# Performance work log

Hardware: AMD Instinct MI355X
Metric: run time of the kernel (lower is better)

Reference implementation:

```python
import jax, jax.numpy as jnp
import numpy as np

N_NODES = 50000
N_EDGES = 800000
D_FEAT = 64


def setup_inputs() -> dict:
    key = jax.random.key(0)
    k1, k2, k3 = jax.random.split(key, 3)
    x_sum = jax.random.normal(k1, (N_NODES, D_FEAT), dtype=jnp.float32)
    x_prod = jax.random.uniform(k2, (N_NODES, D_FEAT), dtype=jnp.float32)
    edge_index = jax.random.randint(k3, (2, N_EDGES), 0, N_NODES, dtype=jnp.int64)
    return {"x_sum": x_sum, "x_prod": x_prod, "edge_index": edge_index}


def reference(x_sum, x_prod, edge_index):
    # flow='source_to_target' -> gather from edge_index[0], aggregate at edge_index[1]
    src_idx = edge_index[0]
    dst_idx = edge_index[1]
    n = x_sum.shape[0]

    # __lift__: index_select along node dim (message is identity; edge_attr/norm None)
    m_sum = x_sum[src_idx]    # [E, D]
    m_prod = x_prod[src_idx]  # [E, D]

    # scatter_sum: zeros-init + scatter_add_
    out_sum = jax.ops.segment_sum(m_sum, dst_idx, num_segments=n)

    # scatter_product: ones-init + scatter_(reduce='multiply')
    out_prod = jnp.ones((n, x_prod.shape[1]), dtype=x_prod.dtype).at[dst_idx].multiply(m_prod)

    return out_sum, out_prod
```

## Files before the change

### kernel.cpp

```cpp
#include <hip/hip_runtime.h>
#include <hip/hip_fp16.h>

#define N_NODES 50000
#define N_EDGES 800000
#define D_FEAT  64
#define BSHIFT  6
#define NBKT    782
#define NB      256
#define CHUNK   3125
#define PSHIFT  20
#define SRC_MASK ((1 << PSHIFT) - 1)

#define WS_FLAG    0
#define WS_TOT     64
#define WS_COFF    (WS_TOT + NBKT)
#define WS_BH      (WS_COFF + NBKT + 1)
#define WS_OFFS    (WS_BH + NBKT * NB)
#define WS_PAIR    (WS_OFFS + N_NODES + 1)
#define WS_SSRC    (WS_PAIR + N_EDGES)
#define WS_PACKED  (WS_SSRC + N_EDGES)
#define WS_INTS    (WS_PACKED + N_NODES * D_FEAT)

__device__ inline void detect_idx_layout(const int* idx, int* flag) {
    int allzero = 1;
    #pragma unroll
    for (int i = 1; i < 129; i += 2) {
        if (idx[i] != 0) allzero = 0;
    }
    *flag = allzero;
}

__global__ __launch_bounds__(256) void init_cast(int* __restrict__ W,
                                                 const int* __restrict__ idx,
                                                 const float* __restrict__ xs,
                                                 const float* __restrict__ xp) {
    int tid = blockIdx.x * blockDim.x + threadIdx.x;
    int stride = gridDim.x * blockDim.x;
    __half2* packed = (__half2*)(W + WS_PACKED);
    const int total = N_NODES * D_FEAT;
    for (int i = tid; i < total; i += stride)
        packed[i] = __floats2half2_rn(xs[i], xp[i]);
    if (tid == 0) {
        detect_idx_layout(idx, W + WS_FLAG);
        W[WS_OFFS + N_NODES] = N_EDGES;
    }
}

__global__ __launch_bounds__(256) void block_hist(const int* __restrict__ idx,
                                                  int* __restrict__ W) {
    __shared__ int h[NBKT];
    for (int i = threadIdx.x; i < NBKT; i += 256) h[i] = 0;
    __syncthreads();
    const int flg = W[WS_FLAG];
    const int base = blockIdx.x * CHUNK;
    for (int e = base + threadIdx.x; e < base + CHUNK; e += 256) {
        int dst = flg ? idx[2 * (N_EDGES + e)] : idx[N_EDGES + e];
        atomicAdd(&h[dst >> BSHIFT], 1);
    }
    __syncthreads();
    for (int i = threadIdx.x; i < NBKT; i += 256)
        W[WS_BH + i * NB + blockIdx.x] = h[i];
}

__global__ __launch_bounds__(256) void bucket_scan(int* __restrict__ W) {
    __shared__ int part[NB];
    int j = blockIdx.x;
    int t = threadIdx.x;
    int c = W[WS_BH + j * NB + t];
    part[t] = c;
    __syncthreads();
    for (int off = 1; off < NB; off <<= 1) {
        int u = (t >= off) ? part[t - off] : 0;
        __syncthreads();
        part[t] += u;
        __syncthreads();
    }
    W[WS_BH + j * NB + t] = part[t] - c;
    if (t == NB - 1) W[WS_TOT + j] = part[t];
}

__global__ __launch_bounds__(1024) void base_scan(int* __restrict__ W) {
    __shared__ int part[1024];
    int t = threadIdx.x;
    int v = (t < NBKT) ? W[WS_TOT + t] : 0;
    part[t] = v;
    __syncthreads();
    for (int off = 1; off < 1024; off <<= 1) {
        int u = (t >= off) ? part[t - off] : 0;
        __syncthreads();
        part[t] += u;
        __syncthreads();
    }
    if (t < NBKT) W[WS_COFF + t] = part[t] - v;
    if (t == 0) W[WS_COFF + NBKT] = N_EDGES;
}

__global__ __launch_bounds__(256) void coarse_scatter(const int* __restrict__ idx,
                                                      int* __restrict__ W) {
    __shared__ int cur[NBKT];
    for (int i = threadIdx.x; i < NBKT; i += 256)
        cur[i] = W[WS_COFF + i] + W[WS_BH + i * NB + blockIdx.x];
    __syncthreads();
    const int flg = W[WS_FLAG];
    const int base = blockIdx.x * CHUNK;
    for (int e = base + threadIdx.x; e < base + CHUNK; e += 256) {
        int src, dst;
        if (flg) { src = idx[2 * e]; dst = idx[2 * (N_EDGES + e)]; }
        else     { src = idx[e];     dst = idx[N_EDGES + e]; }
        int pos = atomicAdd(&cur[dst >> BSHIFT], 1);
        W[WS_PAIR + pos] = src | ((dst & 63) << PSHIFT);
    }
}

__global__ __launch_bounds__(256) void fine_sort(int* __restrict__ W) {
    __shared__ int h[64];
    int b = blockIdx.x;
    int t = threadIdx.x;
    int bbase = W[WS_COFF + b];
    int bend  = W[WS_COFF + b + 1];
    if (t < 64) h[t] = 0;
    __syncthreads();
    for (int e = bbase + t; e < bend; e += 256)
        atomicAdd(&h[(unsigned)W[WS_PAIR + e] >> PSHIFT], 1);
    __syncthreads();
    if (t < 64) {
        int c = h[t];
        int incl = c;
        #pragma unroll
        for (int off = 1; off < 64; off <<= 1) {
            int u = __shfl_up(incl, off, 64);
            if (t >= off) incl += u;
        }
        int excl = incl - c;
        int node = (b << BSHIFT) + t;
        if (node < N_NODES) W[WS_OFFS + node] = bbase + excl;
        h[t] = excl;
    }
    __syncthreads();
    for (int e = bbase + t; e < bend; e += 256) {
        int v = W[WS_PAIR + e];
        int p = atomicAdd(&h[(unsigned)v >> PSHIFT], 1);
        W[WS_SSRC + bbase + p] = v & SRC_MASK;
    }
}

__global__ __launch_bounds__(256) void gather_reduce(const int* __restrict__ W,
                                                     float* __restrict__ out) {
    int wave = (int)((blockIdx.x * blockDim.x + threadIdx.x) >> 6);
    int lane = threadIdx.x & 63;
    if (wave >= N_NODES) return;
    int beg = __builtin_amdgcn_readfirstlane(W[WS_OFFS + wave]);
    int end = __builtin_amdgcn_readfirstlane(W[WS_OFFS + wave + 1]);
    const int* ssrc = W + WS_SSRC;
    const __half2* packed = (const __half2*)(W + WS_PACKED);

    float s0 = 0.f, s1 = 0.f, s2 = 0.f, s3 = 0.f;
    float s4 = 0.f, s5 = 0.f, s6 = 0.f, s7 = 0.f;
    float p0 = 1.f, p1 = 1.f, p2 = 1.f, p3 = 1.f;
    float p4 = 1.f, p5 = 1.f, p6 = 1.f, p7 = 1.f;
    int i = beg;
    for (; i + 7 < end; i += 8) {
        int a0 = ssrc[i],     a1 = ssrc[i + 1], a2 = ssrc[i + 2], a3 = ssrc[i + 3];
        int a4 = ssrc[i + 4], a5 = ssrc[i + 5], a6 = ssrc[i + 6], a7 = ssrc[i + 7];
        float2 f0 = __half22float2(packed[a0 * D_FEAT + lane]);
        float2 f1 = __half22float2(packed[a1 * D_FEAT + lane]);
        float2 f2 = __half22float2(packed[a2 * D_FEAT + lane]);
        float2 f3 = __half22float2(packed[a3 * D_FEAT + lane]);
        float2 f4 = __half22float2(packed[a4 * D_FEAT + lane]);
        float2 f5 = __half22float2(packed[a5 * D_FEAT + lane]);
        float2 f6 = __half22float2(packed[a6 * D_FEAT + lane]);
        float2 f7 = __half22float2(packed[a7 * D_FEAT + lane]);
        s0 += f0.x; s1 += f1.x; s2 += f2.x; s3 += f3.x;
        s4 += f4.x; s5 += f5.x; s6 += f6.x; s7 += f7.x;
        p0 *= f0.y; p1 *= f1.y; p2 *= f2.y; p3 *= f3.y;
        p4 *= f4.y; p5 *= f5.y; p6 *= f6.y; p7 *= f7.y;
    }
    for (; i + 1 < end; i += 2) {
        int a0 = ssrc[i], a1 = ssrc[i + 1];
        float2 f0 = __half22float2(packed[a0 * D_FEAT + lane]);
        float2 f1 = __half22float2(packed[a1 * D_FEAT + lane]);
        s0 += f0.x; s1 += f1.x;
        p0 *= f0.y; p1 *= f1.y;
    }
    if (i < end) {
        float2 f = __half22float2(packed[ssrc[i] * D_FEAT + lane]);
        s0 += f.x;
        p0 *= f.y;
    }
    float ssum = ((s0 + s1) + (s2 + s3)) + ((s4 + s5) + (s6 + s7));
    float pprd = ((p0 * p1) * (p2 * p3)) * ((p4 * p5) * (p6 * p7));
    out[(long)wave * D_FEAT + lane] = ssum;
    out[(long)N_NODES * D_FEAT + (long)wave * D_FEAT + lane] = pprd;
}

__device__ inline void atomicMulF32(float* addr, float val) {
    unsigned int* ua = (unsigned int*)addr;
    unsigned int old = __hip_atomic_load(ua, __ATOMIC_RELAXED, __HIP_MEMORY_SCOPE_AGENT);
    while (true) {
        unsigned int assumed = old;
        unsigned int desired = __float_as_uint(__uint_as_float(assumed) * val);
        old = atomicCAS(ua, assumed, desired);
        if (old == assumed) break;
    }
}

__global__ void fb_init(float* __restrict__ out, int* __restrict__ flag,
                        const int* __restrict__ idx) {
    const int n4 = (N_NODES * D_FEAT) / 4;
    int tid = blockIdx.x * blockDim.x + threadIdx.x;
    int stride = gridDim.x * blockDim.x;
    float4* o = (float4*)out;
    const float4 z = make_float4(0.f, 0.f, 0.f, 0.f);
    const float4 one = make_float4(1.f, 1.f, 1.f, 1.f);
    for (int i = tid; i < n4; i += stride) { o[i] = z; o[n4 + i] = one; }
    if (blockIdx.x == 0 && threadIdx.x == 0) detect_idx_layout(idx, flag);
}

__global__ void fb_scatter(const float* __restrict__ xs, const float* __restrict__ xp,
                           const int* __restrict__ idx, float* __restrict__ out,
                           const int* __restrict__ flag) {
    long tid = (long)blockIdx.x * blockDim.x + threadIdx.x;
    const long total = (long)N_EDGES * (D_FEAT / 4);
    if (tid >= total) return;
    int e = (int)(tid >> 4);
    int c = (int)(tid & 15);
    int src, dst;
    if (*flag) { src = idx[2 * e]; dst = idx[2 * (N_EDGES + e)]; }
    else       { src = idx[e];     dst = idx[N_EDGES + e]; }
    const float4 s = ((const float4*)(xs + (long)src * D_FEAT))[c];
    const float4 p = ((const float4*)(xp + (long)src * D_FEAT))[c];
    float* os = out + (long)dst * D_FEAT + c * 4;
    float* op = out + (long)N_NODES * D_FEAT + (long)dst * D_FEAT + c * 4;
    atomicAdd(os + 0, s.x); atomicAdd(os + 1, s.y);
    atomicAdd(os + 2, s.z); atomicAdd(os + 3, s.w);
    atomicMulF32(op + 0, p.x); atomicMulF32(op + 1, p.y);
    atomicMulF32(op + 2, p.z); atomicMulF32(op + 3, p.w);
}

extern "C" void kernel_launch(void* const* d_in, const int* in_sizes, int n_in,
                              void* d_out, int out_size, void* d_ws, size_t ws_size,
                              hipStream_t stream) {
    const float* x_sum  = (const float*)d_in[0];
    const float* x_prod = (const float*)d_in[1];
    const int*   eidx   = (const int*)d_in[2];
    float* out = (float*)d_out;
    int* W = (int*)d_ws;

    if (ws_size < (size_t)WS_INTS * sizeof(int)) {
        fb_init<<<1024, 256, 0, stream>>>(out, W, eidx);
        const long total = (long)N_EDGES * (D_FEAT / 4);
        int grid = (int)((total + 255) / 256);
        fb_scatter<<<grid, 256, 0, stream>>>(x_sum, x_prod, eidx, out, W);
        return;
    }

    init_cast<<<1024, 256, 0, stream>>>(W, eidx, x_sum, x_prod);
    block_hist<<<NB, 256, 0, stream>>>(eidx, W);
    bucket_scan<<<NBKT, 256, 0, stream>>>(W);
    base_scan<<<1, 1024, 0, stream>>>(W);
    coarse_scatter<<<NB, 256, 0, stream>>>(eidx, W);
    fine_sort<<<NBKT, 256, 0, stream>>>(W);
    gather_reduce<<<(N_NODES + 3) / 4, 256, 0, stream>>>(W, out);
}
```

Baseline: 148.2 us.

## Fuse fp16 cast into histogram kernel, per-wave fine-sort histograms, deeper gather unroll

Merges the init_cast and block_hist kernels into a single cast_hist launch. Each block now casts its own chunk of features and computes the layout flag locally, which removes one kernel launch and the dependency on a flag written by a previous kernel. fine_sort switches to four per-wave shared histograms to reduce LDS atomic contention, with offsets derived by prefix over the waves. gather_reduce unrolls to 16 loads in flight per iteration to raise memory-level parallelism, at the cost of more registers and a cast phase that now runs on only 256 blocks.

```diff
diff --git a/kernel.cpp b/kernel.cpp
--- a/kernel.cpp
+++ b/kernel.cpp
@@ -8,6 +8,7 @@
 #define NBKT    782
 #define NB      256
 #define CHUNK   3125
+#define CAST_CHUNK 12500
 #define PSHIFT  20
 #define SRC_MASK ((1 << PSHIFT) - 1)
 
@@ -21,45 +22,43 @@
 #define WS_PACKED  (WS_SSRC + N_EDGES)
 #define WS_INTS    (WS_PACKED + N_NODES * D_FEAT)
 
-__device__ inline void detect_idx_layout(const int* idx, int* flag) {
+__device__ inline int detect_idx_layout_local(const int* idx) {
     int allzero = 1;
     #pragma unroll
     for (int i = 1; i < 129; i += 2) {
         if (idx[i] != 0) allzero = 0;
     }
-    *flag = allzero;
-}
-
-__global__ __launch_bounds__(256) void init_cast(int* __restrict__ W,
+    return allzero;
+}
+
+__global__ __launch_bounds__(256) void cast_hist(int* __restrict__ W,
                                                  const int* __restrict__ idx,
                                                  const float* __restrict__ xs,
                                                  const float* __restrict__ xp) {
-    int tid = blockIdx.x * blockDim.x + threadIdx.x;
-    int stride = gridDim.x * blockDim.x;
-    __half2* packed = (__half2*)(W + WS_PACKED);
-    const int total = N_NODES * D_FEAT;
-    for (int i = tid; i < total; i += stride)
-        packed[i] = __floats2half2_rn(xs[i], xp[i]);
-    if (tid == 0) {
-        detect_idx_layout(idx, W + WS_FLAG);
-        W[WS_OFFS + N_NODES] = N_EDGES;
-    }
-}
-
-__global__ __launch_bounds__(256) void block_hist(const int* __restrict__ idx,
-                                                  int* __restrict__ W) {
     __shared__ int h[NBKT];
     for (int i = threadIdx.x; i < NBKT; i += 256) h[i] = 0;
     __syncthreads();
-    const int flg = W[WS_FLAG];
+
+    const int flg = detect_idx_layout_local(idx);
+    const int t = threadIdx.x;
+
+    __half2* packed = (__half2*)(W + WS_PACKED);
+    const int cbase = blockIdx.x * CAST_CHUNK;
+    for (int i = cbase + t; i < cbase + CAST_CHUNK; i += 256)
+        packed[i] = __floats2half2_rn(xs[i], xp[i]);
+
     const int base = blockIdx.x * CHUNK;
-    for (int e = base + threadIdx.x; e < base + CHUNK; e += 256) {
+    for (int e = base + t; e < base + CHUNK; e += 256) {
         int dst = flg ? idx[2 * (N_EDGES + e)] : idx[N_EDGES + e];
         atomicAdd(&h[dst >> BSHIFT], 1);
     }
     __syncthreads();
-    for (int i = threadIdx.x; i < NBKT; i += 256)
+    for (int i = t; i < NBKT; i += 256)
         W[WS_BH + i * NB + blockIdx.x] = h[i];
+    if (blockIdx.x == 0 && t == 0) {
+        W[WS_FLAG] = flg;
+        W[WS_OFFS + N_NODES] = N_EDGES;
+    }
 }
 
 __global__ __launch_bounds__(256) void bucket_scan(int* __restrict__ W) {
@@ -113,33 +112,39 @@
 }
 
 __global__ __launch_bounds__(256) void fine_sort(int* __restrict__ W) {
-    __shared__ int h[64];
+    __shared__ int h[4][64];
     int b = blockIdx.x;
     int t = threadIdx.x;
+    int w = t >> 6;
+    int lane = t & 63;
     int bbase = W[WS_COFF + b];
     int bend  = W[WS_COFF + b + 1];
-    if (t < 64) h[t] = 0;
+    h[w][lane] = 0;
     __syncthreads();
     for (int e = bbase + t; e < bend; e += 256)
-        atomicAdd(&h[(unsigned)W[WS_PAIR + e] >> PSHIFT], 1);
+        atomicAdd(&h[w][(unsigned)W[WS_PAIR + e] >> PSHIFT], 1);
     __syncthreads();
     if (t < 64) {
-        int c = h[t];
-        int incl = c;
+        int c0 = h[0][t], c1 = h[1][t], c2 = h[2][t], c3 = h[3][t];
+        int tot = c0 + c1 + c2 + c3;
+        int incl = tot;
         #pragma unroll
         for (int off = 1; off < 64; off <<= 1) {
             int u = __shfl_up(incl, off, 64);
             if (t >= off) incl += u;
         }
-        int excl = incl - c;
+        int excl = incl - tot;
         int node = (b << BSHIFT) + t;
         if (node < N_NODES) W[WS_OFFS + node] = bbase + excl;
-        h[t] = excl;
+        h[0][t] = excl;
+        h[1][t] = excl + c0;
+        h[2][t] = excl + c0 + c1;
+        h[3][t] = excl + c0 + c1 + c2;
     }
     __syncthreads();
     for (int e = bbase + t; e < bend; e += 256) {
         int v = W[WS_PAIR + e];
-        int p = atomicAdd(&h[(unsigned)v >> PSHIFT], 1);
+        int p = atomicAdd(&h[w][(unsigned)v >> PSHIFT], 1);
         W[WS_SSRC + bbase + p] = v & SRC_MASK;
     }
 }
@@ -159,30 +164,29 @@
     float p0 = 1.f, p1 = 1.f, p2 = 1.f, p3 = 1.f;
     float p4 = 1.f, p5 = 1.f, p6 = 1.f, p7 = 1.f;
     int i = beg;
-    for (; i + 7 < end; i += 8) {
-        int a0 = ssrc[i],     a1 = ssrc[i + 1], a2 = ssrc[i + 2], a3 = ssrc[i + 3];
-        int a4 = ssrc[i + 4], a5 = ssrc[i + 5], a6 = ssrc[i + 6], a7 = ssrc[i + 7];
-        float2 f0 = __half22float2(packed[a0 * D_FEAT + lane]);
-        float2 f1 = __half22float2(packed[a1 * D_FEAT + lane]);
-        float2 f2 = __half22float2(packed[a2 * D_FEAT + lane]);
-        float2 f3 = __half22float2(packed[a3 * D_FEAT + lane]);
-        float2 f4 = __half22float2(packed[a4 * D_FEAT + lane]);
-        float2 f5 = __half22float2(packed[a5 * D_FEAT + lane]);
-        float2 f6 = __half22float2(packed[a6 * D_FEAT + lane]);
-        float2 f7 = __half22float2(packed[a7 * D_FEAT + lane]);
+    for (; i + 15 < end; i += 16) {
+        float2 f[16];
+        #pragma unroll
+        for (int k = 0; k < 16; ++k)
+            f[k] = __half22float2(packed[ssrc[i + k] * D_FEAT + lane]);
+        s0 += f[0].x + f[8].x;  s1 += f[1].x + f[9].x;
+        s2 += f[2].x + f[10].x; s3 += f[3].x + f[11].x;
+        s4 += f[4].x + f[12].x; s5 += f[5].x + f[13].x;
+        s6 += f[6].x + f[14].x; s7 += f[7].x + f[15].x;
+        p0 *= f[0].y * f[8].y;  p1 *= f[1].y * f[9].y;
+        p2 *= f[2].y * f[10].y; p3 *= f[3].y * f[11].y;
+        p4 *= f[4].y * f[12].y; p5 *= f[5].y * f[13].y;
+        p6 *= f[6].y * f[14].y; p7 *= f[7].y * f[15].y;
+    }
+    for (; i + 3 < end; i += 4) {
+        float2 f0 = __half22float2(packed[ssrc[i] * D_FEAT + lane]);
+        float2 f1 = __half22float2(packed[ssrc[i + 1] * D_FEAT + lane]);
+        float2 f2 = __half22float2(packed[ssrc[i + 2] * D_FEAT + lane]);
+        float2 f3 = __half22float2(packed[ssrc[i + 3] * D_FEAT + lane]);
         s0 += f0.x; s1 += f1.x; s2 += f2.x; s3 += f3.x;
-        s4 += f4.x; s5 += f5.x; s6 += f6.x; s7 += f7.x;
         p0 *= f0.y; p1 *= f1.y; p2 *= f2.y; p3 *= f3.y;
-        p4 *= f4.y; p5 *= f5.y; p6 *= f6.y; p7 *= f7.y;
-    }
-    for (; i + 1 < end; i += 2) {
-        int a0 = ssrc[i], a1 = ssrc[i + 1];
-        float2 f0 = __half22float2(packed[a0 * D_FEAT + lane]);
-        float2 f1 = __half22float2(packed[a1 * D_FEAT + lane]);
-        s0 += f0.x; s1 += f1.x;
-        p0 *= f0.y; p1 *= f1.y;
-    }
-    if (i < end) {
+    }
+    for (; i < end; ++i) {
         float2 f = __half22float2(packed[ssrc[i] * D_FEAT + lane]);
         s0 += f.x;
         p0 *= f.y;
@@ -213,7 +217,7 @@
     const float4 z = make_float4(0.f, 0.f, 0.f, 0.f);
     const float4 one = make_float4(1.f, 1.f, 1.f, 1.f);
     for (int i = tid; i < n4; i += stride) { o[i] = z; o[n4 + i] = one; }
-    if (blockIdx.x == 0 && threadIdx.x == 0) detect_idx_layout(idx, flag);
+    if (blockIdx.x == 0 && threadIdx.x == 0) *flag = detect_idx_layout_local(idx);
 }
 
 __global__ void fb_scatter(const float* __restrict__ xs, const float* __restrict__ xp,
@@ -254,8 +258,7 @@
         return;
     }
 
-    init_cast<<<1024, 256, 0, stream>>>(W, eidx, x_sum, x_prod);
-    block_hist<<<NB, 256, 0, stream>>>(eidx, W);
+    cast_hist<<<NB, 256, 0, stream>>>(W, eidx, x_sum, x_prod);
     bucket_scan<<<NBKT, 256, 0, stream>>>(W);
     base_scan<<<1, 1024, 0, stream>>>(W);
     coarse_scatter<<<NB, 256, 0, stream>>>(eidx, W);
```

Result: slower. 154.1 us (+4.0%).
